# Kernel tuning notes

Measured on AMD Instinct MI355X. Metric: run time of the kernel, lower is better.

Reference implementation:

```python
import jax, jax.numpy as jnp
import numpy as np

B, D, N, K = 4, 1024, 2048, 1024
INIT_STD = 0.05  # keras 'random_normal' initializer default stddev


def setup_inputs() -> dict:
    key = jax.random.key(0)
    kx, kq, kk, kv, ko = jax.random.split(key, 5)
    inputs = jax.random.normal(kx, (B, D, N), dtype=jnp.float32)
    W_Q = jax.random.normal(kq, (K, D), dtype=jnp.float32) * INIT_STD
    W_K = jax.random.normal(kk, (K, D), dtype=jnp.float32) * INIT_STD
    W_V = jax.random.normal(kv, (K, D), dtype=jnp.float32) * INIT_STD
    W_O = jax.random.normal(ko, (K, D), dtype=jnp.float32) * INIT_STD
    return {"inputs": inputs, "W_Q": W_Q, "W_K": W_K, "W_V": W_V, "W_O": W_O}


def reference(inputs, W_Q, W_K, W_V, W_O):
    # inputs: (b, d, n) -- feature-major layout, sequence on the last axis.
    b, d, n = inputs.shape
    # Q/K projections fused into a single bilinear form: (W_Q x_i) . (W_K x_j)
    # logits[b, i, j] = x[:, i]^T W_Q^T W_K x[:, j]
    q = jnp.einsum('kd,bdi->bki', W_Q, inputs)          # (b, k, n)
    kk = jnp.einsum('kd,bdj->bkj', W_K, inputs)         # (b, k, n)
    logits = jnp.einsum('bki,bkj->bij', q, kk)          # (b, n, n)
    # Causal mask D: -inf strictly above the diagonal (query i attends j <= i).
    causal = jnp.tril(jnp.ones((n, n), dtype=bool))
    logits = jnp.where(causal, logits, -jnp.inf)
    A = jax.nn.softmax(logits, axis=-1)                 # (b, n_q, n_k)
    # context[:, :, i] = sum_t x[:, :, t] * A[i, t]
    ctx = jnp.einsum('bet,bit->bei', inputs, A)         # (b, d, n)
    # Residual + fused V/O projection: x + W_O^T W_V x A
    out = inputs + jnp.einsum('kd,ke,bei->bdi', W_O, W_V, ctx)
    return out
```

## Files before the change

kernel.cpp:

```cpp
#include <hip/hip_runtime.h>
#include <hip/hip_bf16.h>
#include <math.h>

#define BB 4
#define DD 1024
#define NN 2048
#define KK 1024
#define NT128 16
#define NTRI 136
#define TRI_ELEMS 16384

typedef __attribute__((ext_vector_type(4))) float f32x4;
typedef __attribute__((ext_vector_type(8))) short bfrag;

typedef __attribute__((address_space(1))) const unsigned int gu32;
typedef __attribute__((address_space(3))) unsigned int lu32;

__device__ __forceinline__ void async16(const void* g, void* l) {
  __builtin_amdgcn_global_load_lds((gu32*)g, (lu32*)l, 16, 0, 0);
}

__device__ __forceinline__ ushort f2b(float f) {
  union { float f; unsigned u; } c; c.f = f;
  unsigned u = c.u + 0x7fffu + ((c.u >> 16) & 1u);
  return (ushort)(u >> 16);
}
__device__ __forceinline__ float b2f(ushort h) {
  union { unsigned u; float f; } c; c.u = ((unsigned)h) << 16;
  return c.f;
}

__global__ __launch_bounds__(256) void prep(
    const float* __restrict__ x,
    const float* __restrict__ WQ, const float* __restrict__ WK,
    const float* __restrict__ WV, const float* __restrict__ WO,
    ushort* __restrict__ xhi, ushort* __restrict__ xTh, ushort* __restrict__ xTl,
    ushort* __restrict__ qh, ushort* __restrict__ ql,
    ushort* __restrict__ kh, ushort* __restrict__ kl_,
    ushort* __restrict__ vh, ushort* __restrict__ oh) {
  const int z = blockIdx.z;
  const int tx = threadIdx.x, ty = threadIdx.y;
  __shared__ float tile[32][33];
  if (z < 4) {
    const int b = z;
    const int n0 = blockIdx.x * 32, d0 = blockIdx.y * 32;
    const float* xb = x + (long)b * DD * NN;
    ushort* xhb = xhi + (long)b * DD * NN;
#pragma unroll
    for (int r = 0; r < 4; ++r) {
      const int dl = ty + r * 8;
      const float v = xb[(long)(d0 + dl) * NN + n0 + tx];
      tile[dl][tx] = v;
      xhb[(long)(d0 + dl) * NN + n0 + tx] = f2b(v);
    }
    __syncthreads();
#pragma unroll
    for (int r = 0; r < 4; ++r) {
      const int nl = ty + r * 8;
      const float v = tile[tx][nl];
      const ushort h = f2b(v);
      const long o = (long)b * NN * DD + (long)(n0 + nl) * DD + d0 + tx;
      xTh[o] = h;
      xTl[o] = f2b(v - b2f(h));
    }
  } else {
    const int w = (z - 4) * 2 + (blockIdx.x >> 5);
    const float* W = (w == 0) ? WQ : (w == 1) ? WK : (w == 2) ? WV : WO;
    ushort* Th = (w == 0) ? qh : (w == 1) ? kh : (w == 2) ? vh : oh;
    ushort* Tl = (w == 0) ? ql : (w == 1) ? kl_ : nullptr;
    const int k0 = (blockIdx.x & 31) * 32, d0 = blockIdx.y * 32;
#pragma unroll
    for (int r = 0; r < 4; ++r) {
      const int kl = ty + r * 8;
      tile[kl][tx] = W[(long)(k0 + kl) * DD + d0 + tx];
    }
    __syncthreads();
#pragma unroll
    for (int r = 0; r < 4; ++r) {
      const int dl = ty + r * 8;
      const float v = tile[tx][dl];
      const ushort h = f2b(v);
      const long o = (long)(d0 + dl) * KK + k0 + tx;
      Th[o] = h;
      if (Tl) Tl[o] = f2b(v - b2f(h));
    }
  }
}

__global__ __launch_bounds__(256) void gemm_w(
    const ushort* __restrict__ qh, const ushort* __restrict__ ql,
    const ushort* __restrict__ kh, const ushort* __restrict__ kl_,
    const ushort* __restrict__ vh, const ushort* __restrict__ oh,
    ushort* __restrict__ mqk_h, ushort* __restrict__ mqk_l,
    ushort* __restrict__ mov_h) {
  extern __shared__ ushort smem[];
  ushort* sAh = smem;
  ushort* sAl = smem + 2048;
  ushort* sBh = smem + 4096;
  ushort* sBl = smem + 6144;

  const int id = blockIdx.x;
  const int half = id >> 8;
  const int t = id & 255;
  const int m0 = (t >> 4) * 64, n0 = (t & 15) * 64;
  const ushort* A_h = half ? oh : qh;
  const ushort* B_h = half ? vh : kh;

  const int tid = threadIdx.x;
  const int lane = tid & 63, wave = tid >> 6;
  const int wm = (wave & 1) * 32, wn = (wave >> 1) * 32;
  const int r16 = lane & 15, quad = lane >> 4;
  const int kc = ((lane & 3) ^ ((lane >> 3) & 3)) * 8;
  const int srow = lane >> 2;

  f32x4 acc[2][2];
#pragma unroll
  for (int i = 0; i < 2; ++i)
#pragma unroll
    for (int j = 0; j < 2; ++j) acc[i][j] = (f32x4){0.f, 0.f, 0.f, 0.f};

  for (int k0 = 0; k0 < KK; k0 += 32) {
    __syncthreads();
    {
      const int row = wave * 16 + srow;
      const long aoff = (long)(m0 + row) * KK + k0 + kc;
      const long boff = (long)(n0 + row) * KK + k0 + kc;
      async16(A_h + aoff, sAh + wave * 512);
      async16(B_h + boff, sBh + wave * 512);
      if (half == 0) {
        async16(ql + aoff, sAl + wave * 512);
        async16(kl_ + boff, sBl + wave * 512);
      }
    }
    __syncthreads();

    const int sw = (r16 >> 1) & 3;
    bfrag ah[2], bh[2], al[2], bl[2];
#pragma unroll
    for (int t2 = 0; t2 < 2; ++t2) {
      ah[t2] = *(const bfrag*)&sAh[(wm + t2 * 16 + r16) * 32 + (quad ^ sw) * 8];
      bh[t2] = *(const bfrag*)&sBh[(wn + t2 * 16 + r16) * 32 + (quad ^ sw) * 8];
      if (half == 0) {
        al[t2] = *(const bfrag*)&sAl[(wm + t2 * 16 + r16) * 32 + (quad ^ sw) * 8];
        bl[t2] = *(const bfrag*)&sBl[(wn + t2 * 16 + r16) * 32 + (quad ^ sw) * 8];
      }
    }
#pragma unroll
    for (int mt = 0; mt < 2; ++mt)
#pragma unroll
      for (int nt = 0; nt < 2; ++nt) {
        acc[mt][nt] = __builtin_amdgcn_mfma_f32_16x16x32_bf16(ah[mt], bh[nt], acc[mt][nt], 0, 0, 0);
        if (half == 0) {
          acc[mt][nt] = __builtin_amdgcn_mfma_f32_16x16x32_bf16(ah[mt], bl[nt], acc[mt][nt], 0, 0, 0);
          acc[mt][nt] = __builtin_amdgcn_mfma_f32_16x16x32_bf16(al[mt], bh[nt], acc[mt][nt], 0, 0, 0);
        }
      }
  }

#pragma unroll
  for (int mt = 0; mt < 2; ++mt)
#pragma unroll
    for (int nt = 0; nt < 2; ++nt)
#pragma unroll
      for (int reg = 0; reg < 4; ++reg) {
        const int ml = wm + mt * 16 + quad * 4 + reg;
        const int nl = wn + nt * 16 + r16;
        const float v = acc[mt][nt][reg];
        const long o = (long)(m0 + ml) * DD + n0 + nl;
        if (half == 0) {
          const ushort h = f2b(v);
          mqk_h[o] = h;
          mqk_l[o] = f2b(v - b2f(h));
        } else {
          mov_h[o] = f2b(v);
        }
      }
}

template <int SPLIT, int TRIA, int STORE, int SWIZ>
__global__ __launch_bounds__(256) void gemm_mfma(
    const ushort* __restrict__ Ah, const ushort* __restrict__ Al,
    const ushort* __restrict__ Bh, const ushort* __restrict__ Bl,
    void* __restrict__ C0, void* __restrict__ C1, const float* __restrict__ Res,
    int K, int lda, int ldb, int ldc,
    long bA, long bB, long bC, long bR) {
  extern __shared__ ushort smem[];
  ushort* sAh = smem;
  ushort* sBh = smem + (SPLIT ? 16384 : 8192);
  ushort* sAl = SPLIT ? smem + 8192 : nullptr;
  ushort* sBl = SPLIT ? smem + 24576 : nullptr;

  int b, m0, n0, tiC = 0;
  if (SWIZ == 2) {
    const int g = (blockIdx.x & 7) * 68 + (blockIdx.x >> 3);
    b = g / NTRI;
    int t = g - b * NTRI;
    int ti = 0;
    while ((ti + 1) * (ti + 2) / 2 <= t) ++ti;
    const int tj = t - ti * (ti + 1) / 2;
    m0 = ti * 128; n0 = tj * 128; tiC = t;
  } else if (SWIZ == 1) {
    const int g = (blockIdx.x & 7) * 64 + (blockIdx.x >> 3);
    const int P = g >> 3;
    b = P >> 4;
    m0 = (P & 15) * 128;
    n0 = (g & 7) * 128;
  } else if (SWIZ == 3) {
    const int xcd = blockIdx.x & 7;
    const int idx = blockIdx.x >> 3;
    const int q = idx >> 3;
    b = q >> 1;
    const int mt_ = (q & 1) ? (15 - xcd) : xcd;
    m0 = mt_ * 128;
    n0 = (idx & 7) * 128;
  } else {
    const int g = (blockIdx.x & 7) * 64 + (blockIdx.x >> 3);
    const int P = g >> 3;
    b = P >> 4;
    n0 = (P & 15) * 128;
    m0 = (g & 7) * 128;
  }
  const int kmax = TRIA ? (m0 + 128) : K;
  int triA0 = 0;
  if (TRIA) { const int ti = m0 >> 7; triA0 = ti * (ti + 1) / 2; }

  const ushort* A_h = Ah + (long)b * bA;
  const ushort* B_h = Bh + (long)b * bB;
  const ushort* A_l = SPLIT ? Al + (long)b * bA : nullptr;
  const ushort* B_l = SPLIT ? Bl + (long)b * bB : nullptr;

  const int tid = threadIdx.x;
  const int lane = tid & 63, wave = tid >> 6;
  const int wm = (wave & 1) * 64, wn = (wave >> 1) * 64;
  const int r16 = lane & 15, quad = lane >> 4;
  const int kc = ((lane & 7) ^ (lane >> 3)) * 8;
  const int lrow = lane >> 3;

  f32x4 acc[4][4];
#pragma unroll
  for (int i = 0; i < 4; ++i)
#pragma unroll
    for (int j = 0; j < 4; ++j) acc[i][j] = (f32x4){0.f, 0.f, 0.f, 0.f};

  for (int k0 = 0; k0 < kmax; k0 += 64) {
    __syncthreads();
    {
#pragma unroll
      for (int c = 0; c < 4; ++c) {
        const int seg = wave * 4 + c;
        const int row = seg * 8 + lrow;
        long aoff;
        if (TRIA)
          aoff = (long)(triA0 + (k0 >> 7)) * TRI_ELEMS + (long)row * 128 + (k0 & 127) + kc;
        else
          aoff = (long)(m0 + row) * lda + k0 + kc;
        const long boff = (long)(n0 + row) * ldb + k0 + kc;
        async16(A_h + aoff, sAh + seg * 512);
        async16(B_h + boff, sBh + seg * 512);
        if (SPLIT) {
          async16(A_l + aoff, sAl + seg * 512);
          async16(B_l + boff, sBl + seg * 512);
        }
      }
    }
    __syncthreads();

    const int sw = r16 & 7;
#pragma unroll
    for (int ksub = 0; ksub < 2; ++ksub) {
      const int ch = ((ksub * 4 + quad) ^ sw) * 8;
      bfrag ah[4], bh[4], al[4], bl[4];
#pragma unroll
      for (int t4 = 0; t4 < 4; ++t4) {
        ah[t4] = *(const bfrag*)&sAh[(wm + t4 * 16 + r16) * 64 + ch];
        bh[t4] = *(const bfrag*)&sBh[(wn + t4 * 16 + r16) * 64 + ch];
        if (SPLIT) {
          al[t4] = *(const bfrag*)&sAl[(wm + t4 * 16 + r16) * 64 + ch];
          bl[t4] = *(const bfrag*)&sBl[(wn + t4 * 16 + r16) * 64 + ch];
        }
      }
#pragma unroll
      for (int mt = 0; mt < 4; ++mt)
#pragma unroll
        for (int nt = 0; nt < 4; ++nt) {
          acc[mt][nt] = __builtin_amdgcn_mfma_f32_16x16x32_bf16(ah[mt], bh[nt], acc[mt][nt], 0, 0, 0);
          if (SPLIT) {
            acc[mt][nt] = __builtin_amdgcn_mfma_f32_16x16x32_bf16(ah[mt], bl[nt], acc[mt][nt], 0, 0, 0);
            acc[mt][nt] = __builtin_amdgcn_mfma_f32_16x16x32_bf16(al[mt], bh[nt], acc[mt][nt], 0, 0, 0);
          }
        }
    }
  }

#pragma unroll
  for (int mt = 0; mt < 4; ++mt)
#pragma unroll
    for (int nt = 0; nt < 4; ++nt)
#pragma unroll
      for (int reg = 0; reg < 4; ++reg) {
        const int ml = wm + mt * 16 + quad * 4 + reg;
        const int nl = wn + nt * 16 + r16;
        const float v = acc[mt][nt][reg];
        if (STORE == 0) {
          ushort* Ch = (ushort*)C0 + (long)b * bC;
          ushort* Cl = (ushort*)C1 + (long)b * bC;
          const long o = (long)(m0 + ml) * ldc + n0 + nl;
          const ushort h = f2b(v);
          Ch[o] = h;
          Cl[o] = f2b(v - b2f(h));
        } else if (STORE == 1) {
          float* C = (float*)C0 + (long)b * bC + (long)tiC * TRI_ELEMS;
          C[ml * 128 + nl] = v;
        } else if (STORE == 2) {
          ushort* C = (ushort*)C0 + (long)b * bC;
          C[(long)(m0 + ml) * ldc + n0 + nl] = f2b(v);
        } else {
          float* C = (float*)C0 + (long)b * bC;
          const float* R = Res + (long)b * bR;
          const long o = (long)(m0 + ml) * ldc + n0 + nl;
          C[o] = R[o] + v;
        }
      }
}

__global__ __launch_bounds__(256) void softmax_tri(
    const float* __restrict__ L, ushort* __restrict__ Aout) {
  const int row = blockIdx.x;
  const int b = row >> 11, i = row & (NN - 1);
  const int ti = i >> 7, ml = i & 127;
  const long base = (long)b * ((long)NTRI * TRI_ELEMS);
  const int trib = ti * (ti + 1) / 2;
  const int len = i + 1;
  const int tot = (ti + 1) * 128;
  const int tid = threadIdx.x;
  __shared__ float red[256];
  float vv[8];
  float m = -INFINITY;
#pragma unroll
  for (int u = 0; u < 8; ++u) {
    const int j = tid + u * 256;
    if (j < len) {
      const float v = L[base + (long)(trib + (j >> 7)) * TRI_ELEMS + ml * 128 + (j & 127)];
      vv[u] = v;
      m = fmaxf(m, v);
    }
  }
  red[tid] = m; __syncthreads();
  for (int s = 128; s; s >>= 1) { if (tid < s) red[tid] = fmaxf(red[tid], red[tid + s]); __syncthreads(); }
  m = red[0]; __syncthreads();
  float sum = 0.f;
#pragma unroll
  for (int u = 0; u < 8; ++u) {
    const int j = tid + u * 256;
    if (j < len) { const float e = __expf(vv[u] - m); vv[u] = e; sum += e; }
  }
  red[tid] = sum; __syncthreads();
  for (int s = 128; s; s >>= 1) { if (tid < s) red[tid] += red[tid + s]; __syncthreads(); }
  const float inv = 1.f / red[0];
#pragma unroll
  for (int u = 0; u < 8; ++u) {
    const int j = tid + u * 256;
    if (j < tot) {
      const ushort o = (j < len) ? f2b(vv[u] * inv) : (ushort)0;
      Aout[base + (long)(trib + (j >> 7)) * TRI_ELEMS + ml * 128 + (j & 127)] = o;
    }
  }
}

extern "C" void kernel_launch(void* const* d_in, const int* in_sizes, int n_in,
                              void* d_out, int out_size, void* d_ws, size_t ws_size,
                              hipStream_t stream) {
  const float* x = (const float*)d_in[0];
  const float* WQ = (const float*)d_in[1];
  const float* WK = (const float*)d_in[2];
  const float* WV = (const float*)d_in[3];
  const float* WO = (const float*)d_in[4];
  float* out = (float*)d_out;

  const long XE = (long)BB * DD * NN;
  const long WE = (long)DD * KK;
  ushort* x_hi = (ushort*)d_ws;
  ushort* xTh = x_hi + XE;
  ushort* xTl = xTh + XE;
  ushort* wqT_h = xTl + XE;
  ushort* wqT_l = wqT_h + WE;
  ushort* wkT_h = wqT_l + WE;
  ushort* wkT_l = wkT_h + WE;
  ushort* wvT_h = wkT_l + WE;
  ushort* woT_h = wvT_h + WE;
  ushort* mqk_h = woT_h + WE;
  ushort* mqk_l = mqk_h + WE;
  ushort* mov_h = mqk_l + WE;
  ushort* tTh = mov_h + WE;
  ushort* tTl = tTh + XE;
  float* logits = (float*)(tTl + XE);
  ushort* A_tri = tTh;
  ushort* ctxT = (ushort*)logits;
  const long TRIB = (long)NTRI * TRI_ELEMS;
  const long XB = XE / BB;

  prep<<<dim3(64, 32, 6), dim3(32, 8), 0, stream>>>(
      x, WQ, WK, WV, WO, x_hi, xTh, xTl,
      wqT_h, wqT_l, wkT_h, wkT_l, wvT_h, woT_h);

  gemm_w<<<dim3(512), 256, 16384, stream>>>(
      wqT_h, wqT_l, wkT_h, wkT_l, wvT_h, woT_h, mqk_h, mqk_l, mov_h);

  gemm_mfma<1, 0, 0, 1><<<dim3(512), 256, 65536, stream>>>(
      xTh, xTl, mqk_h, mqk_l, tTh, tTl, nullptr,
      DD, DD, DD, DD, XB, 0, XB, 0);

  gemm_mfma<1, 0, 1, 2><<<dim3(BB * NTRI), 256, 65536, stream>>>(
      xTh, xTl, tTh, tTl, logits, nullptr, nullptr,
      DD, DD, DD, 0, XB, XB, TRIB, 0);

  softmax_tri<<<dim3(BB * NN), 256, 0, stream>>>(logits, A_tri);

  gemm_mfma<0, 1, 2, 3><<<dim3(512), 256, 32768, stream>>>(
      A_tri, nullptr, x_hi, nullptr, ctxT, nullptr, nullptr,
      NN, 0, NN, DD, TRIB, XB, XB, 0);

  gemm_mfma<0, 0, 3, 4><<<dim3(512), 256, 32768, stream>>>(
      mov_h, nullptr, ctxT, nullptr, out, nullptr, x,
      DD, DD, DD, NN, 0, XB, XB, XB);
}
```

Baseline: 344.0 us.

## Double-buffer GEMM K-loop with 32-wide stages and async prefetch two ahead

Replaces the single-buffered 64-wide K step with a two-stage LDS double buffer holding 32-wide K slices. Loads for stage t+2 are issued after the current fragments are read, and explicit vmcnt waits let global-to-LDS copies overlap the MFMA work. The LDS swizzle is redone for 32-element rows. The cost is an extra barrier per iteration and half the MFMA work per sync, and the hand-written waitcnt values must match the number of outstanding loads.

```diff
diff --git a/kernel.cpp b/kernel.cpp
--- a/kernel.cpp
+++ b/kernel.cpp
@@ -185,10 +185,8 @@
     int K, int lda, int ldb, int ldc,
     long bA, long bB, long bC, long bR) {
   extern __shared__ ushort smem[];
-  ushort* sAh = smem;
-  ushort* sBh = smem + (SPLIT ? 16384 : 8192);
-  ushort* sAl = SPLIT ? smem + 8192 : nullptr;
-  ushort* sBl = SPLIT ? smem + 24576 : nullptr;
+  constexpr int DBS = SPLIT ? 16384 : 8192;
+  constexpr int BO  = SPLIT ? 8192  : 4096;
 
   int b, m0, n0, tiC = 0;
   if (SWIZ == 2) {
@@ -233,8 +231,10 @@
   const int lane = tid & 63, wave = tid >> 6;
   const int wm = (wave & 1) * 64, wn = (wave >> 1) * 64;
   const int r16 = lane & 15, quad = lane >> 4;
-  const int kc = ((lane & 7) ^ (lane >> 3)) * 8;
-  const int lrow = lane >> 3;
+
+  const int srow = lane >> 2;
+  const int fsw = ((lane >> 4) & 1) | (srow & 2);
+  const int kc = ((lane & 3) ^ fsw) * 8;
 
   f32x4 acc[4][4];
 #pragma unroll
@@ -242,54 +242,72 @@
 #pragma unroll
     for (int j = 0; j < 4; ++j) acc[i][j] = (f32x4){0.f, 0.f, 0.f, 0.f};
 
-  for (int k0 = 0; k0 < kmax; k0 += 64) {
-    __syncthreads();
-    {
-#pragma unroll
-      for (int c = 0; c < 4; ++c) {
-        const int seg = wave * 4 + c;
-        const int row = seg * 8 + lrow;
-        long aoff;
-        if (TRIA)
-          aoff = (long)(triA0 + (k0 >> 7)) * TRI_ELEMS + (long)row * 128 + (k0 & 127) + kc;
-        else
-          aoff = (long)(m0 + row) * lda + k0 + kc;
-        const long boff = (long)(n0 + row) * ldb + k0 + kc;
-        async16(A_h + aoff, sAh + seg * 512);
-        async16(B_h + boff, sBh + seg * 512);
+  const int T = kmax >> 5;
+
+  auto STAGE = [&](int db, int t) {
+    const int k0 = t << 5;
+    ushort* dst = smem + db * DBS;
+#pragma unroll
+    for (int h = 0; h < 2; ++h) {
+      const int row = wave * 32 + h * 16 + srow;
+      long aoff;
+      if (TRIA)
+        aoff = (long)(triA0 + (k0 >> 7)) * TRI_ELEMS + (long)row * 128 + (k0 & 127) + kc;
+      else
+        aoff = (long)(m0 + row) * lda + k0 + kc;
+      const long boff = (long)(n0 + row) * ldb + k0 + kc;
+      const int d0 = wave * 1024 + h * 512;
+      async16(A_h + aoff, dst + d0);
+      async16(B_h + boff, dst + BO + d0);
+      if (SPLIT) {
+        async16(A_l + aoff, dst + 4096 + d0);
+        async16(B_l + boff, dst + 12288 + d0);
+      }
+    }
+  };
+
+  STAGE(0, 0);
+  STAGE(1, 1);
+
+  const int fr = ((r16 >> 2) & 1) | (r16 & 2);
+  const int pc8 = (quad ^ fr) * 8;
+
+  for (int t = 0; t < T; ++t) {
+    const int db = t & 1;
+    if (t + 1 < T) {
+      if (SPLIT) asm volatile("s_waitcnt vmcnt(8)" ::: "memory");
+      else       asm volatile("s_waitcnt vmcnt(4)" ::: "memory");
+    } else {
+      asm volatile("s_waitcnt vmcnt(0)" ::: "memory");
+    }
+    __builtin_amdgcn_s_barrier();
+
+    const ushort* src = smem + db * DBS;
+    bfrag ah[4], bh[4], al[4], bl[4];
+#pragma unroll
+    for (int t4 = 0; t4 < 4; ++t4) {
+      ah[t4] = *(const bfrag*)&src[(wm + t4 * 16 + r16) * 32 + pc8];
+      bh[t4] = *(const bfrag*)&src[BO + (wn + t4 * 16 + r16) * 32 + pc8];
+      if (SPLIT) {
+        al[t4] = *(const bfrag*)&src[4096 + (wm + t4 * 16 + r16) * 32 + pc8];
+        bl[t4] = *(const bfrag*)&src[12288 + (wn + t4 * 16 + r16) * 32 + pc8];
+      }
+    }
+    if (t + 2 < T) {
+      asm volatile("s_waitcnt lgkmcnt(0)" ::: "memory");
+      __builtin_amdgcn_s_barrier();
+      STAGE(db, t + 2);
+    }
+#pragma unroll
+    for (int mt = 0; mt < 4; ++mt)
+#pragma unroll
+      for (int nt = 0; nt < 4; ++nt) {
+        acc[mt][nt] = __builtin_amdgcn_mfma_f32_16x16x32_bf16(ah[mt], bh[nt], acc[mt][nt], 0, 0, 0);
         if (SPLIT) {
-          async16(A_l + aoff, sAl + seg * 512);
-          async16(B_l + boff, sBl + seg * 512);
+          acc[mt][nt] = __builtin_amdgcn_mfma_f32_16x16x32_bf16(ah[mt], bl[nt], acc[mt][nt], 0, 0, 0);
+          acc[mt][nt] = __builtin_amdgcn_mfma_f32_16x16x32_bf16(al[mt], bh[nt], acc[mt][nt], 0, 0, 0);
         }
       }
-    }
-    __syncthreads();
-
-    const int sw = r16 & 7;
-#pragma unroll
-    for (int ksub = 0; ksub < 2; ++ksub) {
-      const int ch = ((ksub * 4 + quad) ^ sw) * 8;
-      bfrag ah[4], bh[4], al[4], bl[4];
-#pragma unroll
-      for (int t4 = 0; t4 < 4; ++t4) {
-        ah[t4] = *(const bfrag*)&sAh[(wm + t4 * 16 + r16) * 64 + ch];
-        bh[t4] = *(const bfrag*)&sBh[(wn + t4 * 16 + r16) * 64 + ch];
-        if (SPLIT) {
-          al[t4] = *(const bfrag*)&sAl[(wm + t4 * 16 + r16) * 64 + ch];
-          bl[t4] = *(const bfrag*)&sBl[(wn + t4 * 16 + r16) * 64 + ch];
-        }
-      }
-#pragma unroll
-      for (int mt = 0; mt < 4; ++mt)
-#pragma unroll
-        for (int nt = 0; nt < 4; ++nt) {
-          acc[mt][nt] = __builtin_amdgcn_mfma_f32_16x16x32_bf16(ah[mt], bh[nt], acc[mt][nt], 0, 0, 0);
-          if (SPLIT) {
-            acc[mt][nt] = __builtin_amdgcn_mfma_f32_16x16x32_bf16(ah[mt], bl[nt], acc[mt][nt], 0, 0, 0);
-            acc[mt][nt] = __builtin_amdgcn_mfma_f32_16x16x32_bf16(al[mt], bh[nt], acc[mt][nt], 0, 0, 0);
-          }
-        }
-    }
   }
 
 #pragma unroll
```

Measured after the change: 350.5 us. No clear change (+1.9%).

## Replace split-bf16 projection and logits GEMMs with 256x128-tile 512-thread kernel

Applied to the files above, without the earlier changes.

Adds a new gemm_split8 kernel with 256x128 output tiles, 8 waves per block and a 64x64 sub-tile per wave. It loads hi and lo bf16 halves together into a swizzled, double-buffered LDS layout and runs three MFMAs per fragment pair to emulate higher precision. It uses s_setprio around the MFMA bursts and remaps block indices across XCDs. The causal logits GEMM uses 256-row triangular tiles and writes only the lower-triangle 128x128 blocks. The goal is more data reuse per LDS load and fewer blocks, at the cost of higher register pressure and some wasted work on the diagonal tiles.

```diff
diff --git a/kernel.cpp b/kernel.cpp
--- a/kernel.cpp
+++ b/kernel.cpp
@@ -173,6 +173,146 @@
           mqk_l[o] = f2b(v - b2f(h));
         } else {
           mov_h[o] = f2b(v);
+        }
+      }
+}
+
+template <int MODE>
+__global__ __launch_bounds__(512, 2) void gemm_split8(
+    const ushort* __restrict__ Ah, const ushort* __restrict__ Al,
+    const ushort* __restrict__ Bh, const ushort* __restrict__ Bl,
+    void* __restrict__ C0, void* __restrict__ C1,
+    int lda, int ldb, int ldc, long bA, long bB, long bC) {
+  __shared__ ushort smem[49152];
+
+  int b, m0, n0, tj = 0;
+  if (MODE == 0) {
+    const int g = (blockIdx.x & 7) * 32 + (blockIdx.x >> 3);
+    const int I = g >> 3;
+    b = I >> 3;
+    m0 = (I & 7) * 256;
+    n0 = (g & 7) * 128;
+  } else {
+    const int g = (blockIdx.x & 7) * 36 + (blockIdx.x >> 3);
+    b = g / 72;
+    const int r = g - b * 72;
+    int I = 0;
+    while ((I + 1) * (I + 2) <= r) ++I;
+    const int jt = r - I * (I + 1);
+    m0 = I * 256;
+    n0 = jt * 128;
+    tj = jt;
+  }
+
+  const ushort* A_h = Ah + (long)b * bA;
+  const ushort* A_l = Al + (long)b * bA;
+  const ushort* B_h = Bh + (long)b * bB;
+  const ushort* B_l = Bl + (long)b * bB;
+
+  const int tid = threadIdx.x;
+  const int lane = tid & 63, wave = tid >> 6;
+  const int wm = (wave & 3) * 64, wn = (wave >> 2) * 64;
+  const int r16 = lane & 15, quad = lane >> 4;
+  const int rk = r16 & 7;
+
+  const int lrow = lane >> 3;
+  const int lc = (lane & 7) ^ lrow;
+  const int lck = (lc & 3) * 8;
+  const bool lo_src = lc >= 4;
+
+  f32x4 acc[4][4];
+#pragma unroll
+  for (int i = 0; i < 4; ++i)
+#pragma unroll
+    for (int j = 0; j < 4; ++j) acc[i][j] = (f32x4){0.f, 0.f, 0.f, 0.f};
+
+  auto STAGE = [&](int db, int t) {
+    const int k0 = t << 5;
+    ushort* dst = smem + db * 24576;
+#pragma unroll
+    for (int s = 0; s < 4; ++s) {
+      const int seg = wave * 4 + s;
+      const int row = seg * 8 + lrow;
+      const ushort* base = lo_src ? A_l : A_h;
+      async16(base + (long)(m0 + row) * lda + k0 + lck, dst + seg * 512);
+    }
+#pragma unroll
+    for (int s = 0; s < 2; ++s) {
+      const int seg = wave * 2 + s;
+      const int row = seg * 8 + lrow;
+      const ushort* base = lo_src ? B_l : B_h;
+      async16(base + (long)(n0 + row) * ldb + k0 + lck, dst + 16384 + seg * 512);
+    }
+  };
+
+  const int T = KK >> 5;
+  STAGE(0, 0);
+
+  for (int t = 0; t < T; ++t) {
+    const int db = t & 1;
+    asm volatile("s_waitcnt vmcnt(0)" ::: "memory");
+    __builtin_amdgcn_s_barrier();
+    if (t + 1 < T) STAGE(db ^ 1, t + 1);
+
+    const ushort* sA = smem + db * 24576;
+    const ushort* sB = sA + 16384;
+    bfrag ah[4], al[4], bh[4], bl[4];
+#pragma unroll
+    for (int f = 0; f < 4; ++f) {
+      const int arow = (wm + f * 16 + r16) * 64;
+      const int brow = (wn + f * 16 + r16) * 64;
+      ah[f] = *(const bfrag*)&sA[arow + ((quad ^ rk)) * 8];
+      al[f] = *(const bfrag*)&sA[arow + (((quad + 4) ^ rk)) * 8];
+      bh[f] = *(const bfrag*)&sB[brow + ((quad ^ rk)) * 8];
+      bl[f] = *(const bfrag*)&sB[brow + (((quad + 4) ^ rk)) * 8];
+    }
+
+    __builtin_amdgcn_s_setprio(1);
+#pragma unroll
+    for (int mt = 0; mt < 2; ++mt)
+#pragma unroll
+      for (int nt = 0; nt < 4; ++nt) {
+        acc[mt][nt] = __builtin_amdgcn_mfma_f32_16x16x32_bf16(ah[mt], bh[nt], acc[mt][nt], 0, 0, 0);
+        acc[mt][nt] = __builtin_amdgcn_mfma_f32_16x16x32_bf16(ah[mt], bl[nt], acc[mt][nt], 0, 0, 0);
+        acc[mt][nt] = __builtin_amdgcn_mfma_f32_16x16x32_bf16(al[mt], bh[nt], acc[mt][nt], 0, 0, 0);
+      }
+    __builtin_amdgcn_s_setprio(0);
+    __builtin_amdgcn_s_barrier();
+    __builtin_amdgcn_s_setprio(1);
+#pragma unroll
+    for (int mt = 2; mt < 4; ++mt)
+#pragma unroll
+      for (int nt = 0; nt < 4; ++nt) {
+        acc[mt][nt] = __builtin_amdgcn_mfma_f32_16x16x32_bf16(ah[mt], bh[nt], acc[mt][nt], 0, 0, 0);
+        acc[mt][nt] = __builtin_amdgcn_mfma_f32_16x16x32_bf16(ah[mt], bl[nt], acc[mt][nt], 0, 0, 0);
+        acc[mt][nt] = __builtin_amdgcn_mfma_f32_16x16x32_bf16(al[mt], bh[nt], acc[mt][nt], 0, 0, 0);
+      }
+    __builtin_amdgcn_s_setprio(0);
+  }
+
+#pragma unroll
+  for (int mt = 0; mt < 4; ++mt)
+#pragma unroll
+    for (int nt = 0; nt < 4; ++nt)
+#pragma unroll
+      for (int reg = 0; reg < 4; ++reg) {
+        const int ml = wm + mt * 16 + quad * 4 + reg;
+        const int nl = wn + nt * 16 + r16;
+        const float v = acc[mt][nt][reg];
+        if (MODE == 0) {
+          ushort* Ch = (ushort*)C0 + (long)b * bC;
+          ushort* Cl = (ushort*)C1 + (long)b * bC;
+          const long o = (long)(m0 + ml) * ldc + n0 + nl;
+          const ushort h = f2b(v);
+          Ch[o] = h;
+          Cl[o] = f2b(v - b2f(h));
+        } else {
+          const int gi = m0 + ml;
+          const int ti = gi >> 7;
+          if (tj <= ti) {
+            float* C = (float*)C0 + (long)b * bC;
+            C[(long)(ti * (ti + 1) / 2 + tj) * TRI_ELEMS + (gi & 127) * 128 + nl] = v;
+          }
         }
       }
 }
@@ -406,13 +546,13 @@
   gemm_w<<<dim3(512), 256, 16384, stream>>>(
       wqT_h, wqT_l, wkT_h, wkT_l, wvT_h, woT_h, mqk_h, mqk_l, mov_h);
 
-  gemm_mfma<1, 0, 0, 1><<<dim3(512), 256, 65536, stream>>>(
-      xTh, xTl, mqk_h, mqk_l, tTh, tTl, nullptr,
-      DD, DD, DD, DD, XB, 0, XB, 0);
-
-  gemm_mfma<1, 0, 1, 2><<<dim3(BB * NTRI), 256, 65536, stream>>>(
-      xTh, xTl, tTh, tTl, logits, nullptr, nullptr,
-      DD, DD, DD, 0, XB, XB, TRIB, 0);
+  gemm_split8<0><<<dim3(256), dim3(512), 0, stream>>>(
+      xTh, xTl, mqk_h, mqk_l, tTh, tTl,
+      DD, DD, DD, XB, 0, XB);
+
+  gemm_split8<1><<<dim3(288), dim3(512), 0, stream>>>(
+      xTh, xTl, tTh, tTl, logits, nullptr,
+      DD, DD, 0, XB, XB, TRIB);
 
   softmax_tri<<<dim3(BB * NN), 256, 0, stream>>>(logits, A_tri);
 
```

After: 349.9 us. Within noise of the previous version (+1.7%).

## Double-buffer LDS tiles in MFMA GEMM and repack split hi/lo into one tile

Applied to the files above, without the earlier changes.

Replaces the load-sync-compute loop in the shared GEMM kernel with a two-stage LDS ping-pong: the next K-tile is fetched asynchronously into the alternate buffer while MFMAs run on the current one, with a single waitcnt+barrier per iteration. For the split-precision path, hi and lo halves are packed into the same 64-wide LDS row (32 K each), halving K per stage but unifying the layout. It also raises wave priority around MFMA blocks, and doubles dynamic LDS for the non-split launches, which may reduce occupancy.

```diff
diff --git a/kernel.cpp b/kernel.cpp
--- a/kernel.cpp
+++ b/kernel.cpp
@@ -185,10 +185,6 @@
     int K, int lda, int ldb, int ldc,
     long bA, long bB, long bC, long bR) {
   extern __shared__ ushort smem[];
-  ushort* sAh = smem;
-  ushort* sBh = smem + (SPLIT ? 16384 : 8192);
-  ushort* sAl = SPLIT ? smem + 8192 : nullptr;
-  ushort* sBl = SPLIT ? smem + 24576 : nullptr;
 
   int b, m0, n0, tiC = 0;
   if (SWIZ == 2) {
@@ -233,8 +229,13 @@
   const int lane = tid & 63, wave = tid >> 6;
   const int wm = (wave & 1) * 64, wn = (wave >> 1) * 64;
   const int r16 = lane & 15, quad = lane >> 4;
-  const int kc = ((lane & 7) ^ (lane >> 3)) * 8;
+  const int rk = r16 & 7;
+
   const int lrow = lane >> 3;
+  const int lc = (lane & 7) ^ lrow;
+  const int lckS = (lc & 3) * 8;
+  const bool lo_src = lc >= 4;
+  const int kcP = lc * 8;
 
   f32x4 acc[4][4];
 #pragma unroll
@@ -242,54 +243,93 @@
 #pragma unroll
     for (int j = 0; j < 4; ++j) acc[i][j] = (f32x4){0.f, 0.f, 0.f, 0.f};
 
-  for (int k0 = 0; k0 < kmax; k0 += 64) {
-    __syncthreads();
-    {
-#pragma unroll
-      for (int c = 0; c < 4; ++c) {
-        const int seg = wave * 4 + c;
+  auto STAGE = [&](int db, int t) {
+    ushort* dst = smem + db * 16384;
+    if (SPLIT) {
+      const int k0 = t << 5;
+#pragma unroll
+      for (int s = 0; s < 4; ++s) {
+        const int seg = wave * 4 + s;
+        const int row = seg * 8 + lrow;
+        const ushort* baseA = lo_src ? A_l : A_h;
+        const ushort* baseB = lo_src ? B_l : B_h;
+        async16(baseA + (long)(m0 + row) * lda + k0 + lckS, dst + seg * 512);
+        async16(baseB + (long)(n0 + row) * ldb + k0 + lckS, dst + 8192 + seg * 512);
+      }
+    } else {
+      const int k0 = t << 6;
+#pragma unroll
+      for (int s = 0; s < 4; ++s) {
+        const int seg = wave * 4 + s;
         const int row = seg * 8 + lrow;
         long aoff;
         if (TRIA)
-          aoff = (long)(triA0 + (k0 >> 7)) * TRI_ELEMS + (long)row * 128 + (k0 & 127) + kc;
+          aoff = (long)(triA0 + (k0 >> 7)) * TRI_ELEMS + (long)row * 128 + (k0 & 127) + kcP;
         else
-          aoff = (long)(m0 + row) * lda + k0 + kc;
-        const long boff = (long)(n0 + row) * ldb + k0 + kc;
-        async16(A_h + aoff, sAh + seg * 512);
-        async16(B_h + boff, sBh + seg * 512);
-        if (SPLIT) {
-          async16(A_l + aoff, sAl + seg * 512);
-          async16(B_l + boff, sBl + seg * 512);
-        }
-      }
-    }
-    __syncthreads();
-
-    const int sw = r16 & 7;
-#pragma unroll
-    for (int ksub = 0; ksub < 2; ++ksub) {
-      const int ch = ((ksub * 4 + quad) ^ sw) * 8;
-      bfrag ah[4], bh[4], al[4], bl[4];
-#pragma unroll
-      for (int t4 = 0; t4 < 4; ++t4) {
-        ah[t4] = *(const bfrag*)&sAh[(wm + t4 * 16 + r16) * 64 + ch];
-        bh[t4] = *(const bfrag*)&sBh[(wn + t4 * 16 + r16) * 64 + ch];
-        if (SPLIT) {
-          al[t4] = *(const bfrag*)&sAl[(wm + t4 * 16 + r16) * 64 + ch];
-          bl[t4] = *(const bfrag*)&sBl[(wn + t4 * 16 + r16) * 64 + ch];
-        }
-      }
+          aoff = (long)(m0 + row) * lda + k0 + kcP;
+        async16(A_h + aoff, dst + seg * 512);
+        async16(B_h + (long)(n0 + row) * ldb + k0 + kcP, dst + 8192 + seg * 512);
+      }
+    }
+  };
+
+  const int T = kmax >> (SPLIT ? 5 : 6);
+  STAGE(0, 0);
+  asm volatile("s_waitcnt vmcnt(0)" ::: "memory");
+  __builtin_amdgcn_s_barrier();
+  __builtin_amdgcn_sched_barrier(0);
+
+  for (int t = 0; t < T; ++t) {
+    const int cur = t & 1;
+    if (t + 1 < T) STAGE(cur ^ 1, t + 1);
+    const ushort* sA = smem + cur * 16384;
+    const ushort* sB = sA + 8192;
+
+    if (SPLIT) {
+      bfrag ah[4], al[4], bh[4], bl[4];
+#pragma unroll
+      for (int f = 0; f < 4; ++f) {
+        const int arow = (wm + f * 16 + r16) * 64;
+        const int brow = (wn + f * 16 + r16) * 64;
+        ah[f] = *(const bfrag*)&sA[arow + (quad ^ rk) * 8];
+        al[f] = *(const bfrag*)&sA[arow + ((quad + 4) ^ rk) * 8];
+        bh[f] = *(const bfrag*)&sB[brow + (quad ^ rk) * 8];
+        bl[f] = *(const bfrag*)&sB[brow + ((quad + 4) ^ rk) * 8];
+      }
+      __builtin_amdgcn_s_setprio(1);
 #pragma unroll
       for (int mt = 0; mt < 4; ++mt)
 #pragma unroll
         for (int nt = 0; nt < 4; ++nt) {
           acc[mt][nt] = __builtin_amdgcn_mfma_f32_16x16x32_bf16(ah[mt], bh[nt], acc[mt][nt], 0, 0, 0);
-          if (SPLIT) {
-            acc[mt][nt] = __builtin_amdgcn_mfma_f32_16x16x32_bf16(ah[mt], bl[nt], acc[mt][nt], 0, 0, 0);
-            acc[mt][nt] = __builtin_amdgcn_mfma_f32_16x16x32_bf16(al[mt], bh[nt], acc[mt][nt], 0, 0, 0);
-          }
+          acc[mt][nt] = __builtin_amdgcn_mfma_f32_16x16x32_bf16(ah[mt], bl[nt], acc[mt][nt], 0, 0, 0);
+          acc[mt][nt] = __builtin_amdgcn_mfma_f32_16x16x32_bf16(al[mt], bh[nt], acc[mt][nt], 0, 0, 0);
         }
-    }
+      __builtin_amdgcn_s_setprio(0);
+    } else {
+#pragma unroll
+      for (int ksub = 0; ksub < 2; ++ksub) {
+        const int ch = ((ksub * 4 + quad) ^ rk) * 8;
+        bfrag a4[4], b4[4];
+#pragma unroll
+        for (int f = 0; f < 4; ++f) {
+          a4[f] = *(const bfrag*)&sA[(wm + f * 16 + r16) * 64 + ch];
+          b4[f] = *(const bfrag*)&sB[(wn + f * 16 + r16) * 64 + ch];
+        }
+        __builtin_amdgcn_s_setprio(1);
+#pragma unroll
+        for (int mt = 0; mt < 4; ++mt)
+#pragma unroll
+          for (int nt = 0; nt < 4; ++nt)
+            acc[mt][nt] = __builtin_amdgcn_mfma_f32_16x16x32_bf16(a4[mt], b4[nt], acc[mt][nt], 0, 0, 0);
+        __builtin_amdgcn_s_setprio(0);
+      }
+    }
+
+    __builtin_amdgcn_sched_barrier(0);
+    asm volatile("s_waitcnt vmcnt(0)" ::: "memory");
+    __builtin_amdgcn_s_barrier();
+    __builtin_amdgcn_sched_barrier(0);
   }
 
 #pragma unroll
@@ -416,11 +456,11 @@
 
   softmax_tri<<<dim3(BB * NN), 256, 0, stream>>>(logits, A_tri);
 
-  gemm_mfma<0, 1, 2, 3><<<dim3(512), 256, 32768, stream>>>(
+  gemm_mfma<0, 1, 2, 3><<<dim3(512), 256, 65536, stream>>>(
       A_tri, nullptr, x_hi, nullptr, ctxT, nullptr, nullptr,
       NN, 0, NN, DD, TRIB, XB, XB, 0);
 
-  gemm_mfma<0, 0, 3, 4><<<dim3(512), 256, 32768, stream>>>(
+  gemm_mfma<0, 0, 3, 4><<<dim3(512), 256, 65536, stream>>>(
       mov_h, nullptr, ctxT, nullptr, out, nullptr, x,
       DD, DD, DD, NN, 0, XB, XB, XB);
 }
```

Measured after the change: 327.6 us. -4.7%, faster.
